# Kernel optimization log

Hardware: AMD Instinct MI355X
Metric: run time of the kernel (lower is better)

## Reference

```python
import jax, jax.numpy as jnp
from jax import lax
import numpy as np


def _lap(cost):
    """Jonker-Volgenant shortest-augmenting-path LAP (same optimum as
    scipy.optimize.linear_sum_assignment) on cost [n, m] with n <= m.
    Returns for each row (0..n-1) the assigned column index."""
    n, m = cost.shape
    BIG = jnp.asarray(1e9, cost.dtype)
    a = jnp.pad(cost, ((1, 0), (1, 0)))  # 1-based rows/cols, [n+1, m+1]
    u = jnp.zeros(n + 1, cost.dtype)     # row duals
    v = jnp.zeros(m + 1, cost.dtype)     # col duals
    p = jnp.zeros(m + 1, jnp.int32)      # p[j] = row matched to col j (0 = free)

    def row_step(i, carry):
        u, v, p = carry
        p = p.at[0].set(i)  # virtual col 0 holds the row being inserted
        minv = jnp.full(m + 1, BIG, cost.dtype)
        used = jnp.zeros(m + 1, bool)
        way = jnp.zeros(m + 1, jnp.int32)

        def cond(s):
            u, v, p, way, minv, used, j0 = s
            return p[j0] != 0

        def body(s):
            u, v, p, way, minv, used, j0 = s
            used = used.at[j0].set(True)
            i0 = p[j0]
            cur = a[i0] - u[i0] - v                      # reduced costs, len m+1
            better = (cur < minv) & jnp.logical_not(used)
            minv = jnp.where(better, cur, minv)
            way = jnp.where(better, j0, way)
            masked = jnp.where(used, BIG, minv)
            j1 = jnp.argmin(masked).astype(jnp.int32)
            delta = masked[j1]
            u = u.at[p].add(jnp.where(used, delta, jnp.zeros((), cost.dtype)))
            v = jnp.where(used, v - delta, v)
            minv = jnp.where(used, minv, minv - delta)
            return (u, v, p, way, minv, used, j1)

        u, v, p, way, minv, used, j0 = lax.while_loop(
            cond, body, (u, v, p, way, minv, used, jnp.int32(0)))

        # backtrack the augmenting path
        def cond2(s):
            return s[1] != 0

        def body2(s):
            p, j0 = s
            j1 = way[j0]
            return (p.at[j0].set(p[j1]), j1)

        p, _ = lax.while_loop(cond2, body2, (p, j0))
        return (u, v, p)

    u, v, p = lax.fori_loop(1, n + 1, row_step, (u, v, p))
    # invert: row r (1-based) matched to col j  ->  ans[r-1] = j-1
    cols = jnp.arange(m + 1)
    valid = (p > 0) & (cols > 0)
    idx = jnp.where(valid, p - 1, n)  # invalid entries dumped into scratch slot n
    ans = jnp.zeros(n + 1, jnp.int32).at[idx].set((cols - 1).astype(jnp.int32))
    return ans[:n]


def _cdist_mm(x, y):
    """Batched euclidean cdist via the GEMM trick (torch use_mm_for_euclid_dist)."""
    x2 = jnp.sum(x * x, axis=-1)[..., :, None]   # [B, N, 1]
    y2 = jnp.sum(y * y, axis=-1)[..., None, :]   # [B, 1, M]
    xy = jnp.einsum('bnd,bmd->bnm', x, y)        # [B, N, M]
    return jnp.sqrt(jnp.maximum(x2 + y2 - 2.0 * xy, 0.0))


def setup_inputs() -> dict:
    key = jax.random.key(0)
    k1, k2 = jax.random.split(key)
    outputs = jax.random.normal(k1, (32, 512, 768), dtype=jnp.float32)
    targets = jax.random.normal(k2, (32, 200, 768), dtype=jnp.float32)
    return {"outputs": outputs, "targets": targets}


def reference(outputs, targets):
    # cost[b, n, m] = ||outputs[b, n] - targets[b, m]||_2  (block-diagonal slices
    # of the original cross-batch cdist are all that the matcher consumes)
    cost = _cdist_mm(outputs, targets)                       # [B, N, M]
    # solve with targets as rows (n=M <= m=N): pred column per gt row
    gt_to_pred = jax.vmap(_lap)(jnp.swapaxes(cost, 1, 2))    # [B, M]
    # scipy returns pred indices sorted ascending; replicate that ordering
    order = jnp.argsort(gt_to_pred, axis=1)                  # gt indices (index_j)
    index_i = jnp.take_along_axis(gt_to_pred, order, axis=1)
    index_j = order.astype(jnp.int32)
    return jnp.stack([index_i, index_j], axis=1)             # [B, 2, M] int32
```

## Files before the change

### kernel.cpp

```cpp
#include <hip/hip_runtime.h>
#include <math.h>

static constexpr int BATCH = 32;
static constexpr int NPRED = 512;
static constexpr int NTGT  = 200;
static constexpr int DIM   = 768;
#define BIGF 1e9f
#define QNANF __int_as_float(0x7fc00000)

__global__ __launch_bounds__(64) void norms_kernel(const float* __restrict__ O,
                                                   const float* __restrict__ T,
                                                   float* __restrict__ no_arr,
                                                   float* __restrict__ nt_arr) {
    int row = blockIdx.x;
    const float* src;
    float* dst;
    if (row < BATCH * NPRED) {
        src = O + (size_t)row * DIM;            dst = no_arr + row;
    } else {
        int r2 = row - BATCH * NPRED;
        src = T + (size_t)r2 * DIM;             dst = nt_arr + r2;
    }
    const float4* r = (const float4*)src;
    float s = 0.f;
#pragma unroll
    for (int k = 0; k < 3; ++k) {
        float4 v = r[threadIdx.x + 64 * k];
        s += v.x * v.x + v.y * v.y + v.z * v.z + v.w * v.w;
    }
#pragma unroll
    for (int off = 32; off; off >>= 1) s += __shfl_down(s, off);
    if (threadIdx.x == 0) *dst = s;
}

__global__ __launch_bounds__(256) void cost_kernel(const float* __restrict__ O,
                                                   const float* __restrict__ T,
                                                   const float* __restrict__ no_arr,
                                                   const float* __restrict__ nt_arr,
                                                   float* __restrict__ cost) {
    const int wg  = blockIdx.x;
    const int xcd = wg & 7;
    const int idx = wg >> 3;
    const int b   = xcd + 8 * (idx >> 4);
    const int t0  = idx & 15;
    const int n0  = (t0 & 7) * 64;
    const int m0  = (t0 >> 3) * 128;

    const float* Tb = T + (size_t)b * NTGT * DIM;
    const float* Ob = O + (size_t)b * NPRED * DIM;

    __shared__ __align__(16) float As[32][132];
    __shared__ __align__(16) float Bs[32][68];

    const int tid = threadIdx.x;
    const int tx = tid & 15;
    const int ty = tid >> 4;

    int arow[4], akk[4];
    const float* pA[4];
#pragma unroll
    for (int q = 0; q < 4; ++q) {
        int f = tid + q * 256;
        int r = f >> 3;
        int kk = (f & 7) << 2;
        int gm = m0 + r; if (gm > NTGT - 1) gm = NTGT - 1;
        arow[q] = r; akk[q] = kk;
        pA[q] = Tb + (size_t)gm * DIM + kk;
    }
    int brow[2], bkk[2];
    const float* pB[2];
#pragma unroll
    for (int q = 0; q < 2; ++q) {
        int f = tid + q * 256;
        int r = f >> 3;
        int kk = (f & 7) << 2;
        brow[q] = r; bkk[q] = kk;
        pB[q] = Ob + (size_t)(n0 + r) * DIM + kk;
    }

    float4 rA[4], rB[2];
#pragma unroll
    for (int q = 0; q < 4; ++q) rA[q] = *(const float4*)(pA[q]);
#pragma unroll
    for (int q = 0; q < 2; ++q) rB[q] = *(const float4*)(pB[q]);

    float acc[8][4] = {};

    for (int t = 0; t < DIM / 32; ++t) {
#pragma unroll
        for (int q = 0; q < 4; ++q) {
            As[akk[q] + 0][arow[q]] = rA[q].x;
            As[akk[q] + 1][arow[q]] = rA[q].y;
            As[akk[q] + 2][arow[q]] = rA[q].z;
            As[akk[q] + 3][arow[q]] = rA[q].w;
        }
#pragma unroll
        for (int q = 0; q < 2; ++q) {
            Bs[bkk[q] + 0][brow[q]] = rB[q].x;
            Bs[bkk[q] + 1][brow[q]] = rB[q].y;
            Bs[bkk[q] + 2][brow[q]] = rB[q].z;
            Bs[bkk[q] + 3][brow[q]] = rB[q].w;
        }
        __syncthreads();

        if (t + 1 < DIM / 32) {
            int k0n = (t + 1) * 32;
#pragma unroll
            for (int q = 0; q < 4; ++q) rA[q] = *(const float4*)(pA[q] + k0n);
#pragma unroll
            for (int q = 0; q < 2; ++q) rB[q] = *(const float4*)(pB[q] + k0n);
        }

#pragma unroll
        for (int k = 0; k < 32; ++k) {
            float4 a0 = *(const float4*)&As[k][ty * 8];
            float4 a1 = *(const float4*)&As[k][ty * 8 + 4];
            float4 bv = *(const float4*)&Bs[k][tx * 4];
            float av[8] = {a0.x, a0.y, a0.z, a0.w, a1.x, a1.y, a1.z, a1.w};
#pragma unroll
            for (int i = 0; i < 8; ++i) {
                acc[i][0] += av[i] * bv.x; acc[i][1] += av[i] * bv.y;
                acc[i][2] += av[i] * bv.z; acc[i][3] += av[i] * bv.w;
            }
        }
        __syncthreads();
    }

    {
        float4 nov = *(const float4*)(no_arr + b * NPRED + n0 + (tx << 2));
#pragma unroll
        for (int i = 0; i < 8; ++i) {
            int gm = m0 + ty * 8 + i;
            if (gm < NTGT) {
                float ntv = nt_arr[b * NTGT + gm];
                float4 o;
                o.x = sqrtf(fmaxf(ntv + nov.x - 2.0f * acc[i][0], 0.0f));
                o.y = sqrtf(fmaxf(ntv + nov.y - 2.0f * acc[i][1], 0.0f));
                o.z = sqrtf(fmaxf(ntv + nov.z - 2.0f * acc[i][2], 0.0f));
                o.w = sqrtf(fmaxf(ntv + nov.w - 2.0f * acc[i][3], 0.0f));
                *(float4*)&cost[((size_t)b * NTGT + gm) * NPRED + n0 + (tx << 2)] = o;
            }
        }
    }
}

__device__ __forceinline__ int rl(int v, int l) {
    return __builtin_amdgcn_readlane(v, l);
}
__device__ __forceinline__ float rlf(float v, int l) {
    return __int_as_float(__builtin_amdgcn_readlane(__float_as_int(v), l));
}
__device__ __forceinline__ int sel8i(const int* a, int s) {
    int r = a[0];
#pragma unroll
    for (int k = 1; k < 8; ++k) r = (s == k) ? a[k] : r;
    return r;
}
__device__ __forceinline__ float sel8f(const float* a, int s) {
    float r = a[0];
#pragma unroll
    for (int k = 1; k < 8; ++k) r = (s == k) ? a[k] : r;
    return r;
}
__device__ __forceinline__ float dpp_min_f32(float x) {
    float t;
    t = __int_as_float(__builtin_amdgcn_update_dpp(__float_as_int(x), __float_as_int(x), 0x111, 0xF, 0xF, false)); x = fminf(x, t);
    t = __int_as_float(__builtin_amdgcn_update_dpp(__float_as_int(x), __float_as_int(x), 0x112, 0xF, 0xF, false)); x = fminf(x, t);
    t = __int_as_float(__builtin_amdgcn_update_dpp(__float_as_int(x), __float_as_int(x), 0x114, 0xF, 0xF, false)); x = fminf(x, t);
    t = __int_as_float(__builtin_amdgcn_update_dpp(__float_as_int(x), __float_as_int(x), 0x118, 0xF, 0xF, false)); x = fminf(x, t);
    t = __int_as_float(__builtin_amdgcn_update_dpp(__float_as_int(x), __float_as_int(x), 0x142, 0xF, 0xF, false)); x = fminf(x, t);
    t = __int_as_float(__builtin_amdgcn_update_dpp(__float_as_int(x), __float_as_int(x), 0x143, 0xF, 0xF, false)); x = fminf(x, t);
    return x;
}
__device__ __forceinline__ float tree8n(const float* m, int& lq) {
    float v01 = fminf(m[0], m[1]); int q01 = (v01 == m[0]) ? 0 : 1;
    float v23 = fminf(m[2], m[3]); int q23 = (v23 == m[2]) ? 2 : 3;
    float v45 = fminf(m[4], m[5]); int q45 = (v45 == m[4]) ? 4 : 5;
    float v67 = fminf(m[6], m[7]); int q67 = (v67 == m[6]) ? 6 : 7;
    float v03 = fminf(v01, v23);   int q03 = (v03 == v01) ? q01 : q23;
    float v47 = fminf(v45, v67);   int q47 = (v47 == v45) ? q45 : q67;
    float r = fminf(v03, v47);     lq = (r == v03) ? q03 : q47;
    return r;
}

__global__ __launch_bounds__(64) void lap_kernel(const float* __restrict__ cost,
                                                 int* __restrict__ out) {
    const int b = blockIdx.x;
    const int lane = threadIdx.x;
    const float* C = cost + (size_t)b * NTGT * NPRED;
    const float* Cl = C + lane * 8;

    __shared__ float u0[NTGT + 1];
    __shared__ int g2p[NTGT];

    for (int k = lane; k < NTGT + 1; k += 64) u0[k] = 0.f;

    float v[8], minv[8], up[8];
    int p_arr[8], way_arr[8];
#pragma unroll
    for (int q = 0; q < 8; ++q) {
        v[q] = 0.f; up[q] = 0.f; p_arr[q] = 0; way_arr[q] = 0;
    }
    __syncthreads();

    float4 ca = *(const float4*)(Cl);
    float4 cb = *(const float4*)(Cl + 4);
    float4 sa = ca, sb = cb;

    for (int i = 1; i <= NTGT; ++i) {
#pragma unroll
        for (int q = 0; q < 8; ++q) minv[q] = BIGF;
        float uI = 0.f;
        float u_i0 = 0.f;
        int j0 = 0;
        int j1 = 0;
        int spec_j = 0;

        for (int it = 0; it <= NPRED; ++it) {
            float c[8];
            c[0] = ca.x; c[1] = ca.y; c[2] = ca.z; c[3] = ca.w;
            c[4] = cb.x; c[5] = cb.y; c[6] = cb.z; c[7] = cb.w;

            bool used_b[8];
#pragma unroll
            for (int q = 0; q < 8; ++q) {
                used_b[q] = __builtin_isnan(minv[q]);
                float cur = (c[q] - u_i0) - v[q];
                bool imp = cur < minv[q];
                minv[q] = imp ? cur : minv[q];
                way_arr[q] = imp ? j0 : way_arr[q];
            }

            int lq;
            float lval = tree8n(minv, lq);
            int   psel = sel8i(p_arr, lq);
            float usel = sel8f(up, lq);
            float wmin = rlf(dpp_min_f32(lval), 63);
            unsigned long long mask = __ballot(lval == wmin);
            int w = (int)__builtin_ctzll(mask);
            int qw  = rl(lq, w);
            int i0n = rl(psel, w);
            float u_n = rlf(usel, w);
            float delta = wmin;
            j1 = w * 8 + qw + 1;
            bool done = (i0n == 0);

            if (!done) {
                if (j1 == spec_j) {
                    ca = sa; cb = sb;
                } else {
                    const float* Crow = Cl + (size_t)(i0n - 1) * NPRED;
                    ca = *(const float4*)(Crow);
                    cb = *(const float4*)(Crow + 4);
                }
                float lv2 = (lane == w) ? QNANF : lval;
                float wm2 = rlf(dpp_min_f32(lv2), 63);
                unsigned long long m2 = __ballot(lv2 == wm2);
                int w2 = (int)__builtin_ctzll(m2);
                int q2 = rl(lq, w2);
                int p2 = rl(psel, w2);
                int sj = w2 * 8 + q2 + 1;
                if (p2 != 0 && sj != spec_j) {
                    const float* Srow = Cl + (size_t)(p2 - 1) * NPRED;
                    sa = *(const float4*)(Srow);
                    sb = *(const float4*)(Srow + 4);
                }
                spec_j = sj;
            }

            uI += delta;
#pragma unroll
            for (int q = 0; q < 8; ++q) {
                float d0 = used_b[q] ? delta : 0.f;
                v[q]  -= d0;
                up[q] += d0;
                minv[q] -= delta;
            }
            {
                bool lw = (lane == w);
#pragma unroll
                for (int q = 0; q < 8; ++q)
                    minv[q] = (lw && q == qw) ? QNANF : minv[q];
            }

            if (done) break;
            u_i0 = u_n;
            j0 = j1;
        }

        if (i < NTGT) {
            const float* Crow = Cl + (size_t)i * NPRED;
            ca = *(const float4*)(Crow);
            cb = *(const float4*)(Crow + 4);
        }

#pragma unroll
        for (int q = 0; q < 8; ++q) {
            bool usedq = __builtin_isnan(minv[q]);
            if (usedq && p_arr[q] != 0) u0[p_arr[q]] = up[q];
        }
        if (lane == 0) u0[i] = uI;

        {
            int j = j1;
            for (int s = 0; s <= NPRED; ++s) {
                int ow = (j - 1) >> 3, oq = (j - 1) & 7;
                int wj = rl(sel8i(way_arr, oq), ow);
                int pOfW;
                if (wj == 0) {
                    pOfW = i;
                } else {
                    int ow2 = (wj - 1) >> 3, oq2 = (wj - 1) & 7;
                    pOfW = rl(sel8i(p_arr, oq2), ow2);
                }
#pragma unroll
                for (int q = 0; q < 8; ++q) {
                    bool mine = (lane == ow) && (q == oq);
                    p_arr[q] = mine ? pOfW : p_arr[q];
                }
                if (wj == 0) break;
                j = wj;
            }
        }

        __syncthreads();
#pragma unroll
        for (int q = 0; q < 8; ++q) up[q] = u0[p_arr[q]];
    }

#pragma unroll
    for (int q = 0; q < 8; ++q) {
        int r = p_arr[q];
        if (r > 0) g2p[r - 1] = lane * 8 + q;
    }
    __syncthreads();

    for (int t = lane; t < NTGT; t += 64) {
        int myv = g2p[t];
        int rank = 0;
        for (int l = 0; l < NTGT; ++l) rank += (g2p[l] < myv) ? 1 : 0;
        out[b * 2 * NTGT + rank] = myv;
        out[b * 2 * NTGT + NTGT + rank] = t;
    }
}

extern "C" void kernel_launch(void* const* d_in, const int* in_sizes, int n_in,
                              void* d_out, int out_size, void* d_ws, size_t ws_size,
                              hipStream_t stream) {
    const float* outputs = (const float*)d_in[0];
    const float* targets = (const float*)d_in[1];
    int* out = (int*)d_out;

    float* cost   = (float*)d_ws;
    float* no_arr = cost + (size_t)BATCH * NTGT * NPRED;
    float* nt_arr = no_arr + (size_t)BATCH * NPRED;

    norms_kernel<<<BATCH * (NPRED + NTGT), 64, 0, stream>>>(outputs, targets,
                                                            no_arr, nt_arr);
    cost_kernel<<<512, 256, 0, stream>>>(outputs, targets, no_arr, nt_arr, cost);
    lap_kernel<<<BATCH, 64, 0, stream>>>(cost, out);
}
```

Before: 761.8 us.

## Greedy row-min pre-assignment before augmenting only unassigned rows in LAP

Before the shortest-augmenting-path phase, computes each row's minimum and argmin column, assigns rows whose argmin column is not claimed by a lower row, and sets their duals to the row minimum. Only the remaining unassigned rows are then augmented, with the next row's cost slice prefetched by list. This aims to cut the number of serial augmentation iterations. It adds a full pass over the cost matrix and extra shared memory, and changes augmentation order, which could alter tie-breaking.

```diff
diff --git a/kernel.cpp b/kernel.cpp
--- a/kernel.cpp
+++ b/kernel.cpp
@@ -192,8 +192,13 @@
 
     __shared__ float u0[NTGT + 1];
     __shared__ int g2p[NTGT];
+    __shared__ float rmin_s[NTGT];
+    __shared__ int   rarg_s[NTGT];
+    __shared__ int   col2row[NPRED];
+    __shared__ int   ulist[NTGT];
 
     for (int k = lane; k < NTGT + 1; k += 64) u0[k] = 0.f;
+    for (int c = lane; c < NPRED; c += 64) col2row[c] = 0x7fffffff;
 
     float v[8], minv[8], up[8];
     int p_arr[8], way_arr[8];
@@ -201,13 +206,65 @@
     for (int q = 0; q < 8; ++q) {
         v[q] = 0.f; up[q] = 0.f; p_arr[q] = 0; way_arr[q] = 0;
     }
+
+    {
+        float4 fa[4], fb[4];
+#pragma unroll
+        for (int d = 0; d < 4; ++d) {
+            fa[d] = *(const float4*)(Cl + (size_t)d * NPRED);
+            fb[d] = *(const float4*)(Cl + (size_t)d * NPRED + 4);
+        }
+        for (int r = 0; r < NTGT; ++r) {
+            int sl = r & 3;
+            float c8[8] = {fa[sl].x, fa[sl].y, fa[sl].z, fa[sl].w,
+                           fb[sl].x, fb[sl].y, fb[sl].z, fb[sl].w};
+            if (r + 4 < NTGT) {
+                fa[sl] = *(const float4*)(Cl + (size_t)(r + 4) * NPRED);
+                fb[sl] = *(const float4*)(Cl + (size_t)(r + 4) * NPRED + 4);
+            }
+            int lq;
+            float lval = tree8n(c8, lq);
+            float wmin = rlf(dpp_min_f32(lval), 63);
+            unsigned long long mask = __ballot(lval == wmin);
+            int w = (int)__builtin_ctzll(mask);
+            int qw = rl(lq, w);
+            if (lane == 0) { rmin_s[r] = wmin; rarg_s[r] = w * 8 + qw; }
+        }
+    }
     __syncthreads();
 
-    float4 ca = *(const float4*)(Cl);
-    float4 cb = *(const float4*)(Cl + 4);
-    float4 sa = ca, sb = cb;
-
-    for (int i = 1; i <= NTGT; ++i) {
+    for (int r = lane; r < NTGT; r += 64) atomicMin(&col2row[rarg_s[r]], r);
+    __syncthreads();
+#pragma unroll
+    for (int q = 0; q < 8; ++q) {
+        int c = lane * 8 + q;
+        int r0 = col2row[c];
+        if (r0 != 0x7fffffff) {
+            p_arr[q] = r0 + 1;
+            u0[r0 + 1] = rmin_s[r0];
+        }
+    }
+    int nu = 0;
+    for (int r0 = 0; r0 < NTGT; r0 += 64) {
+        int r = r0 + lane;
+        bool un = (r < NTGT) && (col2row[rarg_s[r]] != r);
+        unsigned long long m = __ballot(un);
+        if (un) ulist[nu + (int)__popcll(m & ((1ull << lane) - 1))] = r + 1;
+        nu += (int)__popcll(m);
+    }
+    __syncthreads();
+#pragma unroll
+    for (int q = 0; q < 8; ++q) up[q] = u0[p_arr[q]];
+
+    float4 ca, cb, sa, sb;
+    int Rcur = (nu > 0) ? ulist[0] : 1;
+    ca = *(const float4*)(Cl + (size_t)(Rcur - 1) * NPRED);
+    cb = *(const float4*)(Cl + (size_t)(Rcur - 1) * NPRED + 4);
+    sa = ca; sb = cb;
+
+    for (int kk = 0; kk < nu; ++kk) {
+        const int i = Rcur;
+        const int Rnext = (kk + 1 < nu) ? ulist[kk + 1] : 0;
 #pragma unroll
         for (int q = 0; q < 8; ++q) minv[q] = BIGF;
         float uI = 0.f;
@@ -288,8 +345,8 @@
             j0 = j1;
         }
 
-        if (i < NTGT) {
-            const float* Crow = Cl + (size_t)i * NPRED;
+        if (Rnext) {
+            const float* Crow = Cl + (size_t)(Rnext - 1) * NPRED;
             ca = *(const float4*)(Crow);
             cb = *(const float4*)(Crow + 4);
         }
@@ -326,6 +383,8 @@
         __syncthreads();
 #pragma unroll
         for (int q = 0; q < 8; ++q) up[q] = u0[p_arr[q]];
+
+        Rcur = Rnext;
     }
 
 #pragma unroll
```

Result: slower. 785.4 us (+3.1%).
